# Kernel tuning notes

Hardware: AMD Instinct MI355X
Metric: run time of the kernel (lower is better)

## Reference

```python
import jax, jax.numpy as jnp
import numpy as np

T, B, D, H, DH = 2048, 2, 1024, 16, 64


def _rel_shift(x):
    # x: (Q, R, B, H) -- standard Transformer-XL relative shift via pad/reshape
    Q, R = x.shape[0], x.shape[1]
    zero_pad = jnp.zeros((Q, 1) + x.shape[2:], dtype=x.dtype)
    xp = jnp.concatenate([zero_pad, x], axis=1)          # (Q, R+1, B, H)
    xp = xp.reshape((R + 1, Q) + x.shape[2:])            # (R+1, Q, B, H)
    return xp[1:].reshape(x.shape)                       # (Q, R, B, H)


def setup_inputs() -> dict:
    key = jax.random.key(0)
    ks = jax.random.split(key, 7)
    w = jax.random.normal(ks[0], (T, B, D), dtype=jnp.float32)
    r = jax.random.normal(ks[1], (T, D), dtype=jnp.float32)
    w_qkv = jax.random.normal(ks[2], (3 * H * DH, D), dtype=jnp.float32) * 0.02
    w_r = jax.random.normal(ks[3], (H * DH, D), dtype=jnp.float32) * 0.02
    w_o = jax.random.normal(ks[4], (D, H * DH), dtype=jnp.float32) * 0.02
    r_r_bias = jax.random.normal(ks[5], (H, DH), dtype=jnp.float32) * 0.02
    attn_mask = jax.random.uniform(ks[6], (T, B)) < 0.1
    return {"w": w, "r": r, "w_qkv": w_qkv, "w_r": w_r, "w_o": w_o,
            "r_r_bias": r_r_bias, "attn_mask": attn_mask}


def reference(w, r, w_qkv, w_r, w_o, r_r_bias, attn_mask):
    qlen, bsz, d_model = w.shape
    n_head, d_head = r_r_bias.shape
    rlen = r.shape[0]
    scale = 1.0 / d_head ** 0.5

    heads = jnp.einsum('tbd,ed->tbe', w, w_qkv)           # (T, B, 3*H*DH)
    q, k, v = jnp.split(heads, 3, axis=-1)
    q = q.reshape(qlen, bsz, n_head, d_head)
    k = k.reshape(qlen, bsz, n_head, d_head)
    v = v.reshape(qlen, bsz, n_head, d_head)
    r_head_k = jnp.einsum('rd,ed->re', r, w_r).reshape(rlen, n_head, d_head)

    # NOTE: source uses r_r_bias for BOTH content and position biases
    rq = q + r_r_bias[None, None]                         # (Q, B, H, DH)
    AC = jnp.einsum('qbhd,kbhd->bhqk', rq, k)             # content scores
    BD = jnp.einsum('qbhd,rhd->bhqr', rq, r_head_k)       # position scores

    BD = jnp.transpose(BD, (2, 3, 0, 1))                  # (Q, R, B, H)
    BD = _rel_shift(BD)
    BD = jnp.transpose(BD, (2, 3, 0, 1))                  # (B, H, Q, R)
    BD = BD[:, :, :, :qlen]                               # klen == qlen

    score = (AC + BD) * scale                             # (B, H, Q, K)
    # key-padding mask (K, B) -> broadcast (B, 1, 1, K)
    score = jnp.where(attn_mask.T[:, None, None, :], -jnp.inf, score)

    prob = jax.nn.softmax(score.astype(jnp.float32), axis=-1).astype(score.dtype)
    attn_vec = jnp.einsum('bhqk,kbhd->qbhd', prob, v).reshape(qlen, bsz, n_head * d_head)
    out = jnp.einsum('qbe,de->qbd', attn_vec, w_o)        # (Q, B, D)
    return out, prob
```

## Files before the change

### kernel.cpp

```cpp
#include <hip/hip_runtime.h>
#include <hip/hip_bf16.h>
#include <cstdint>
#include <cstddef>

#define TLEN 2048
#define NB 2
#define DMODEL 1024
#define NH 16
#define NDH 64

typedef unsigned short ushortT;
typedef short bf16x8 __attribute__((ext_vector_type(8)));
typedef float f32x16 __attribute__((ext_vector_type(16)));

__device__ __forceinline__ ushortT f2bf(float f) {
  union { float f; unsigned int u; } x{f};
  unsigned int r = x.u + 0x7fff + ((x.u >> 16) & 1);
  return (ushortT)(r >> 16);
}
__device__ __forceinline__ unsigned int pk2(float lo, float hi) {
  return ((unsigned int)f2bf(hi) << 16) | (unsigned int)f2bf(lo);
}
__device__ __forceinline__ float bf2f(ushortT u) {
  union { unsigned int u; float f; } x;
  x.u = ((unsigned int)u) << 16;
  return x.f;
}

__device__ __forceinline__ void gld_lds16(const void* g, void* l) {
  __builtin_amdgcn_global_load_lds(
      (const __attribute__((address_space(1))) unsigned int*)g,
      (__attribute__((address_space(3))) unsigned int*)l, 16, 0, 0);
}


__global__ __launch_bounds__(256) void cvt_all(
    const float* __restrict__ w, const float* __restrict__ wqkv,
    const float* __restrict__ r, const float* __restrict__ wr,
    const float* __restrict__ wo, ushortT* __restrict__ w_bf,
    ushortT* __restrict__ wqkv_bf, ushortT* __restrict__ r_bf,
    ushortT* __restrict__ wr_bf, ushortT* __restrict__ wo_bf,
    const int* __restrict__ mask, float* __restrict__ mfl,
    ushortT* __restrict__ rkE) {
  const size_t N0 = 1048576, N1 = N0 + 786432, N2 = N1 + 524288,
               N3 = N2 + 262144, N4 = N3 + 262144;
  size_t i = (size_t)blockIdx.x * 256 + threadIdx.x;
  const float* src; ushortT* dst; size_t off;
  if (i < N0)      { src = w;    dst = w_bf;    off = i; }
  else if (i < N1) { src = wqkv; dst = wqkv_bf; off = i - N0; }
  else if (i < N2) { src = r;    dst = r_bf;    off = i - N1; }
  else if (i < N3) { src = wr;   dst = wr_bf;   off = i - N2; }
  else if (i < N4) { src = wo;   dst = wo_bf;   off = i - N3; }
  else {
    size_t k = i - N4;
    if (k < 512) {
      int j = (int)k * 4;
#pragma unroll
      for (int s = 0; s < 4; ++s) {
        mfl[j + s]        = mask[(size_t)(j + s) * NB]     ? 0.f : 1.f;
        mfl[TLEN + j + s] = mask[(size_t)(j + s) * NB + 1] ? 0.f : 1.f;
      }
    } else if (k < 512 + 256) {
      int ii = (int)k - 512; int h = ii >> 4, c = ii & 15;
      ushort4 z; z.x = 0; z.y = 0; z.z = 0; z.w = 0;
      *reinterpret_cast<ushort4*>(rkE + ((size_t)h * 4096 + 2048) * NDH + c * 4) = z;
    }
    return;
  }
  float4 v = reinterpret_cast<const float4*>(src)[off];
  ushort4 o;
  o.x = f2bf(v.x); o.y = f2bf(v.y); o.z = f2bf(v.z); o.w = f2bf(v.w);
  reinterpret_cast<ushort4*>(dst)[off] = o;
}


template <typename Epi>
__global__ __launch_bounds__(256) void gemm_bf16(const ushortT* __restrict__ A,
                                                 const ushortT* __restrict__ B,
                                                 int K, Epi epi) {
  __shared__ ushortT Al[128 * 64];
  __shared__ ushortT Bl[128 * 64];
  const int tid = threadIdx.x;
  const int lane = tid & 63;
  const int wv = tid >> 6;
  const int wm = wv >> 1, wn = wv & 1;
  const int m0 = blockIdx.y * 128;
  const int n0 = blockIdx.x * 128;
  const int r32 = lane & 31;
  const int hh = lane >> 5;

  f32x16 acc[2][2];
#pragma unroll
  for (int i = 0; i < 2; ++i)
#pragma unroll
    for (int j = 0; j < 2; ++j)
#pragma unroll
      for (int e = 0; e < 16; ++e) acc[i][j][e] = 0.f;

  for (int k0 = 0; k0 < K; k0 += 64) {
#pragma unroll
    for (int it = 0; it < 4; ++it) {
      int idx = it * 256 + tid;
      int r = idx >> 3, c = idx & 7;
      int gcol = k0 + ((c ^ (r & 7)) << 3);
      gld_lds16(A + (size_t)(m0 + r) * K + gcol, Al + idx * 8);
      gld_lds16(B + (size_t)(n0 + r) * K + gcol, Bl + idx * 8);
    }
    asm volatile("s_waitcnt vmcnt(0)");
    __syncthreads();
#pragma unroll
    for (int kc = 0; kc < 4; ++kc) {
      int lc = kc * 2 + hh;
      bf16x8 af[2], bfr[2];
#pragma unroll
      for (int f = 0; f < 2; ++f) {
        int ar = wm * 64 + f * 32 + r32;
        af[f] = *(const bf16x8*)(Al + ar * 64 + ((lc ^ (ar & 7)) << 3));
        int br = wn * 64 + f * 32 + r32;
        bfr[f] = *(const bf16x8*)(Bl + br * 64 + ((lc ^ (br & 7)) << 3));
      }
#pragma unroll
      for (int i = 0; i < 2; ++i)
#pragma unroll
        for (int j = 0; j < 2; ++j)
          acc[i][j] = __builtin_amdgcn_mfma_f32_32x32x16_bf16(af[i], bfr[j],
                                                              acc[i][j], 0, 0, 0);
    }
    __syncthreads();
  }

#pragma unroll
  for (int i = 0; i < 2; ++i)
#pragma unroll
    for (int j = 0; j < 2; ++j)
#pragma unroll
      for (int rg = 0; rg < 16; ++rg) {
        int m = m0 + wm * 64 + i * 32 + (rg & 3) + 8 * (rg >> 2) + 4 * hh;
        int n = n0 + wn * 64 + j * 32 + r32;
        epi.store(m, n, acc[i][j][rg]);
      }
}

struct EpiQKV {
  ushortT* qb; ushortT* kb; ushortT* vtb; const float* bias;
  __device__ void store(int m, int n, float val) const {
    int t = m >> 1, b = m & 1;
    int which = n >> 10;
    int h = (n >> 6) & (NH - 1);
    int dh = n & (NDH - 1);
    int bh = b * NH + h;
    if (which == 0)
      qb[((size_t)bh * TLEN + t) * NDH + dh] = f2bf(val + bias[(h << 6) | dh]);
    else if (which == 1)
      kb[((size_t)bh * TLEN + t) * NDH + dh] = f2bf(val);
    else
      vtb[((size_t)bh * NDH + dh) * TLEN + t] = f2bf(val);
  }
};

struct EpiRK {
  ushortT* rkE;
  __device__ void store(int m, int n, float val) const {
    int h = n >> 6, dh = n & 63;
    ushortT v = f2bf(val);
    rkE[((size_t)h * 4096 + m) * NDH + dh] = v;
    if (m <= 2046)
      rkE[((size_t)h * 4096 + m + 2049) * NDH + dh] = v;
  }
};

struct EpiOut {
  float* out;
  __device__ void store(int m, int n, float val) const {
    out[(size_t)m * DMODEL + n] = val;
  }
};


__global__ __launch_bounds__(128) void attn_fast(
    const ushortT* __restrict__ qb, const ushortT* __restrict__ kb,
    const ushortT* __restrict__ vtb, const ushortT* __restrict__ rkE,
    const float* __restrict__ mfl, unsigned int* __restrict__ S,
    float* __restrict__ linv_g, ushortT* __restrict__ av_bf) {
  __shared__ float W[2][64][32];
  __shared__ ushortT KT[2048];
  __shared__ ushortT VT[2048];
  __shared__ ushortT RK[6144];

  const int bh = blockIdx.y;
  const int b = bh >> 4, h = bh & 15;
  const int t = threadIdx.x >> 6;
  const int lane = threadIdx.x & 63;
  const int ql = lane & 31;
  const int hh = lane >> 5;
  const int Q0 = blockIdx.x * 64;
  const int q0 = Q0 + 32 * t;
  const int qg = q0 + ql;

  const ushortT* Qbh = qb + (size_t)bh * TLEN * NDH;
  const ushortT* Kbh = kb + (size_t)bh * TLEN * NDH;
  const ushortT* Vbh = vtb + (size_t)bh * NDH * TLEN;
  const ushortT* Rh  = rkE + (size_t)h * 4096 * NDH;
  const float* mflb  = mfl + (size_t)b * TLEN;
  unsigned int* Sb   = S + (size_t)bh * (TLEN / 2) * TLEN;
  float (*Wp)[32] = W[t];

  auto STAGE = [&](int j0) {
    const int U = 1984 + j0 - Q0;
#pragma unroll
    for (int i = 0; i < 6; ++i) {
      int ci = (t * 6 + i) * 64 + lane;
      int row = ci >> 3, c = ci & 7;
      gld_lds16(Rh + (size_t)(U + row) * NDH + ((c ^ (row & 7)) << 3), RK + ci * 8);
    }
#pragma unroll
    for (int i = 0; i < 2; ++i) {
      int ci = (t * 2 + i) * 64 + lane;
      int row = ci >> 3, c = ci & 7;
      gld_lds16(Kbh + (size_t)(j0 + row) * NDH + ((c ^ (row & 7)) << 3), KT + ci * 8);
      int d = ci >> 2, c2 = ci & 3;
      gld_lds16(Vbh + (size_t)d * TLEN + j0 + ((c2 ^ (d & 3)) << 3), VT + ci * 8);
    }
  };

  bf16x8 Qf[4], Qs[4];
  {
    int r2 = min(qg + 1, TLEN - 1);
#pragma unroll
    for (int c = 0; c < 4; ++c) {
      Qf[c] = *(const bf16x8*)(Qbh + (size_t)qg * NDH + c * 16 + hh * 8);
      Qs[c] = *(const bf16x8*)(Qbh + (size_t)r2 * NDH + c * 16 + hh * 8);
    }
  }

  f32x16 pacc0, pacc1;
#pragma unroll
  for (int i = 0; i < 16; ++i) { pacc0[i] = 0.f; pacc1[i] = 0.f; }
  float l_acc = 0.f;

  STAGE(0);
  asm volatile("s_waitcnt vmcnt(0)");
  __builtin_amdgcn_s_barrier();

  for (int j0 = 0; j0 < TLEN; j0 += 32) {
    float4 mf4[4];
#pragma unroll
    for (int g = 0; g < 4; ++g)
      mf4[g] = *(const float4*)(mflb + j0 + 8 * g + 4 * hh);

    const int R1 = 32 * (1 - t) + ql;
    const int R2 = R1 + 32;
    bf16x8 a1[4], a2[4], ak[4];
#pragma unroll
    for (int c = 0; c < 4; ++c) {
      a1[c] = *(const bf16x8*)(RK + R1 * 64 + (((2 * c + hh) ^ (R1 & 7)) << 3));
      a2[c] = *(const bf16x8*)(RK + R2 * 64 + (((2 * c + hh) ^ (R2 & 7)) << 3));
      ak[c] = *(const bf16x8*)(KT + ql * 64 + (((2 * c + hh) ^ (ql & 7)) << 3));
    }
    bf16x8 vv0[2], vv1[2];
#pragma unroll
    for (int kh = 0; kh < 2; ++kh) {
      vv0[kh] = *(const bf16x8*)(VT + ql * 32 + (((2 * kh + hh) ^ (ql & 3)) << 3));
      vv1[kh] = *(const bf16x8*)(VT + (32 + ql) * 32 + (((2 * kh + hh) ^ (ql & 3)) << 3));
    }
    asm volatile("s_waitcnt lgkmcnt(0)");
    __builtin_amdgcn_s_barrier();

    if (j0 + 32 < TLEN) STAGE(j0 + 32);

    const bool t0w1 = (j0 <= q0);
    const bool t1w1 = (j0 < q0);

    f32x16 facc;
#pragma unroll
    for (int i = 0; i < 16; ++i) facc[i] = 0.f;
    __builtin_amdgcn_s_setprio(1);
#pragma unroll
    for (int c = 0; c < 4; ++c)
      facc = __builtin_amdgcn_mfma_f32_32x32x16_bf16(a1[c], t0w1 ? Qf[c] : Qs[c], facc, 0, 0, 0);
    __builtin_amdgcn_s_setprio(0);
#pragma unroll
    for (int r = 0; r < 16; ++r)
      Wp[(r & 3) + 8 * (r >> 2) + 4 * hh][ql] = facc[r];

#pragma unroll
    for (int i = 0; i < 16; ++i) facc[i] = 0.f;
    __builtin_amdgcn_s_setprio(1);
#pragma unroll
    for (int c = 0; c < 4; ++c)
      facc = __builtin_amdgcn_mfma_f32_32x32x16_bf16(a2[c], t1w1 ? Qf[c] : Qs[c], facc, 0, 0, 0);
    __builtin_amdgcn_s_setprio(0);
#pragma unroll
    for (int r = 0; r < 16; ++r)
      Wp[32 + (r & 3) + 8 * (r >> 2) + 4 * hh][ql] = facc[r];

    f32x16 cacc;
#pragma unroll
    for (int i = 0; i < 16; ++i) cacc[i] = 0.f;
    __builtin_amdgcn_s_setprio(1);
#pragma unroll
    for (int c = 0; c < 4; ++c)
      cacc = __builtin_amdgcn_mfma_f32_32x32x16_bf16(ak[c], Qf[c], cacc, 0, 0, 0);
    __builtin_amdgcn_s_setprio(0);

    float p[16];
#pragma unroll
    for (int r = 0; r < 16; ++r) {
      int jrow = (r & 3) + 8 * (r >> 2) + 4 * hh;
      float bd = Wp[jrow - ql + 31][ql];
      float sc = (cacc[r] + bd) * 0.125f;
      float mv = (&mf4[r >> 2].x)[r & 3];
      float pv = mv * __expf(sc);
      p[r] = pv;
      l_acc += pv;
    }

    unsigned int u[8];
#pragma unroll
    for (int i = 0; i < 8; ++i) u[i] = pk2(p[2 * i], p[2 * i + 1]);

#pragma unroll
    for (int i = 0; i < 8; ++i) {
      int r = 2 * i;
      int jrow = (r & 3) + 8 * (r >> 2) + 4 * hh;
      Sb[(size_t)((j0 + jrow) >> 1) * TLEN + qg] = u[i];
    }

#pragma unroll
    for (int kh = 0; kh < 2; ++kh) {
      unsigned int t0 = (unsigned int)__shfl_xor((int)u[4 * kh + 0], 32);
      unsigned int t1 = (unsigned int)__shfl_xor((int)u[4 * kh + 1], 32);
      unsigned int t2 = (unsigned int)__shfl_xor((int)u[4 * kh + 2], 32);
      unsigned int t3 = (unsigned int)__shfl_xor((int)u[4 * kh + 3], 32);
      unsigned int fr[4];
      fr[0] = hh ? t2 : u[4 * kh + 0];
      fr[1] = hh ? t3 : u[4 * kh + 1];
      fr[2] = hh ? u[4 * kh + 2] : t0;
      fr[3] = hh ? u[4 * kh + 3] : t1;
      bf16x8 pa = *reinterpret_cast<bf16x8*>(fr);
      __builtin_amdgcn_s_setprio(1);
      pacc0 = __builtin_amdgcn_mfma_f32_32x32x16_bf16(pa, kh ? vv0[1] : vv0[0], pacc0, 0, 0, 0);
      pacc1 = __builtin_amdgcn_mfma_f32_32x32x16_bf16(pa, kh ? vv1[1] : vv1[0], pacc1, 0, 0, 0);
      __builtin_amdgcn_s_setprio(0);
    }

    if (j0 + 32 < TLEN) {
      asm volatile("s_waitcnt vmcnt(8)");
      __builtin_amdgcn_s_barrier();
    }
  }

  float lt = l_acc + __shfl_xor(l_acc, 32);
  if (lane < 32) linv_g[(size_t)bh * TLEN + qg] = 1.0f / lt;
  float inv = 1.0f / lt;
#pragma unroll
  for (int r = 0; r < 16; ++r) {
    int qrow = (r & 3) + 8 * (r >> 2) + 4 * hh;
    float iv = __shfl(inv, qrow);
    size_t aoff = ((size_t)(q0 + qrow) * NB + b) * DMODEL + h * NDH;
    av_bf[aoff + ql] = f2bf(pacc0[r] * iv);
    av_bf[aoff + 32 + ql] = f2bf(pacc1[r] * iv);
  }
}


__global__ __launch_bounds__(256) void rescale_t(const unsigned int* __restrict__ S,
                                                 const float* __restrict__ linv_g,
                                                 float* __restrict__ prob) {
  __shared__ unsigned int lds[64][65];
  __shared__ float liv[64];
  const int qt = blockIdx.x;
  const int jt = blockIdx.y;
  const int bh = blockIdx.z;
  const int t = threadIdx.x;

  const unsigned int* Sb = S + ((size_t)bh * (TLEN / 2) + jt * 64) * TLEN + qt * 64;
  {
    int row = t >> 2, c0 = (t & 3) * 16;
#pragma unroll
    for (int k = 0; k < 4; ++k) {
      uint4 v = *reinterpret_cast<const uint4*>(Sb + (size_t)row * TLEN + c0 + k * 4);
      lds[row][c0 + k * 4 + 0] = v.x;
      lds[row][c0 + k * 4 + 1] = v.y;
      lds[row][c0 + k * 4 + 2] = v.z;
      lds[row][c0 + k * 4 + 3] = v.w;
    }
  }
  if (t < 64) liv[t] = linv_g[(size_t)bh * TLEN + qt * 64 + t];
  __syncthreads();

  float* P = prob + ((size_t)bh * TLEN + qt * 64) * TLEN + jt * 128;
#pragma unroll
  for (int k = 0; k < 8; ++k) {
    int idx = k * 256 + t;
    int row = idx >> 5, c4 = idx & 31;
    unsigned int u0 = lds[c4 * 2][row];
    unsigned int u1 = lds[c4 * 2 + 1][row];
    float iv = liv[row];
    float4 o;
    o.x = bf2f((ushortT)(u0 & 0xffff)) * iv;
    o.y = bf2f((ushortT)(u0 >> 16)) * iv;
    o.z = bf2f((ushortT)(u1 & 0xffff)) * iv;
    o.w = bf2f((ushortT)(u1 >> 16)) * iv;
    *reinterpret_cast<float4*>(P + (size_t)row * TLEN + c4 * 4) = o;
  }
}


__global__ __launch_bounds__(256) void attn_fused(
    const ushortT* __restrict__ qb, const ushortT* __restrict__ kb,
    const ushortT* __restrict__ vtb, const ushortT* __restrict__ rkE,
    const float* __restrict__ mfl, float* __restrict__ prob,
    ushortT* __restrict__ av_bf) {
  __shared__ float W[4][64][32];
  __shared__ float sl[4][32];
  __shared__ float linv[64];

  const int bh = blockIdx.y;
  const int b = bh >> 4, h = bh & 15;
  const int wv = threadIdx.x >> 6;
  const int lane = threadIdx.x & 63;
  const int ql = lane & 31;
  const int hh = lane >> 5;
  const int qtile = wv & 1;
  const int jh = wv >> 1;
  const int q0 = blockIdx.x * 64 + qtile * 32;
  const int qg = q0 + ql;

  const ushortT* Qbh = qb + (size_t)bh * TLEN * NDH;
  const ushortT* Kbh = kb + (size_t)bh * TLEN * NDH;
  const ushortT* Vbh = vtb + (size_t)bh * NDH * TLEN;
  const ushortT* Rh  = rkE + (size_t)h * 4096 * NDH;
  const float* mflb  = mfl + (size_t)b * TLEN;
  float (*Wp)[32] = W[wv];

  bf16x8 Qf[4], Qs[4];
  {
    int r2 = min(qg + 1, TLEN - 1);
#pragma unroll
    for (int c = 0; c < 4; ++c) {
      Qf[c] = *(const bf16x8*)(Qbh + (size_t)qg * NDH + c * 16 + hh * 8);
      Qs[c] = *(const bf16x8*)(Qbh + (size_t)r2 * NDH + c * 16 + hh * 8);
    }
  }

  f32x16 pacc0, pacc1;
#pragma unroll
  for (int i = 0; i < 16; ++i) { pacc0[i] = 0.f; pacc1[i] = 0.f; }
  float l_acc = 0.f;

  ushortT* pbrow = (ushortT*)prob + ((size_t)bh * TLEN + qg) * 4096 + 2048;

  const int jbeg = jh * (TLEN / 2);
  const int jend = jbeg + (TLEN / 2);
  for (int j0 = jbeg; j0 < jend; j0 += 32) {
    const int base_t = 2016 + j0 - q0;
    const bool t0w1 = (j0 <= q0);
    const bool t1w1 = (j0 < q0);

    const ushortT* s0 = Rh + (size_t)(base_t + ql) * NDH + hh * 8;
    const ushortT* s1 = Rh + (size_t)(base_t + 32 + ql) * NDH + hh * 8;
    const ushortT* sk = Kbh + (size_t)(j0 + ql) * NDH + hh * 8;
    const ushortT* vrow0 = Vbh + (size_t)ql * TLEN + j0 + 8 * hh;
    const ushortT* vrow1 = Vbh + (size_t)(32 + ql) * TLEN + j0 + 8 * hh;
    bf16x8 rk0[4], rk1[4], kk[4];
#pragma unroll
    for (int c = 0; c < 4; ++c) {
      rk0[c] = *(const bf16x8*)(s0 + c * 16);
      rk1[c] = *(const bf16x8*)(s1 + c * 16);
      kk[c]  = *(const bf16x8*)(sk + c * 16);
    }
    bf16x8 v00 = *(const bf16x8*)(vrow0);
    bf16x8 v01 = *(const bf16x8*)(vrow0 + 16);
    bf16x8 v10 = *(const bf16x8*)(vrow1);
    bf16x8 v11 = *(const bf16x8*)(vrow1 + 16);
    float4 mf4[4];
#pragma unroll
    for (int g = 0; g < 4; ++g)
      mf4[g] = *(const float4*)(mflb + j0 + 8 * g + 4 * hh);

    f32x16 facc;
#pragma unroll
    for (int i = 0; i < 16; ++i) facc[i] = 0.f;
    __builtin_amdgcn_s_setprio(1);
#pragma unroll
    for (int c = 0; c < 4; ++c)
      facc = __builtin_amdgcn_mfma_f32_32x32x16_bf16(rk0[c], t0w1 ? Qf[c] : Qs[c], facc, 0, 0, 0);
    __builtin_amdgcn_s_setprio(0);
#pragma unroll
    for (int r = 0; r < 16; ++r)
      Wp[(r & 3) + 8 * (r >> 2) + 4 * hh][ql] = facc[r];

#pragma unroll
    for (int i = 0; i < 16; ++i) facc[i] = 0.f;
    __builtin_amdgcn_s_setprio(1);
#pragma unroll
    for (int c = 0; c < 4; ++c)
      facc = __builtin_amdgcn_mfma_f32_32x32x16_bf16(rk1[c], t1w1 ? Qf[c] : Qs[c], facc, 0, 0, 0);
    __builtin_amdgcn_s_setprio(0);
#pragma unroll
    for (int r = 0; r < 16; ++r)
      Wp[32 + (r & 3) + 8 * (r >> 2) + 4 * hh][ql] = facc[r];

    f32x16 cacc;
#pragma unroll
    for (int i = 0; i < 16; ++i) cacc[i] = 0.f;
    __builtin_amdgcn_s_setprio(1);
#pragma unroll
    for (int c = 0; c < 4; ++c)
      cacc = __builtin_amdgcn_mfma_f32_32x32x16_bf16(kk[c], Qf[c], cacc, 0, 0, 0);
    __builtin_amdgcn_s_setprio(0);

    float p[16];
#pragma unroll
    for (int r = 0; r < 16; ++r) {
      int jrow = (r & 3) + 8 * (r >> 2) + 4 * hh;
      float bd = Wp[jrow - ql + 31][ql];
      float sc = (cacc[r] + bd) * 0.125f;
      float mv = (&mf4[r >> 2].x)[r & 3];
      float pv = mv * __expf(sc);
      p[r] = pv;
      l_acc += pv;
    }

#pragma unroll
    for (int g = 0; g < 4; ++g) {
      uint2 st;
      st.x = pk2(p[4 * g + 0], p[4 * g + 1]);
      st.y = pk2(p[4 * g + 2], p[4 * g + 3]);
      *reinterpret_cast<uint2*>(pbrow + j0 + 8 * g + 4 * hh) = st;
    }

#pragma unroll
    for (int kh = 0; kh < 2; ++kh) {
      unsigned int u0 = pk2(p[8 * kh + 0], p[8 * kh + 1]);
      unsigned int u1 = pk2(p[8 * kh + 2], p[8 * kh + 3]);
      unsigned int u2 = pk2(p[8 * kh + 4], p[8 * kh + 5]);
      unsigned int u3 = pk2(p[8 * kh + 6], p[8 * kh + 7]);
      unsigned int t0 = (unsigned int)__shfl_xor((int)u0, 32);
      unsigned int t1 = (unsigned int)__shfl_xor((int)u1, 32);
      unsigned int t2 = (unsigned int)__shfl_xor((int)u2, 32);
      unsigned int t3 = (unsigned int)__shfl_xor((int)u3, 32);
      unsigned int fr[4];
      fr[0] = hh ? t2 : u0;
      fr[1] = hh ? t3 : u1;
      fr[2] = hh ? u2 : t0;
      fr[3] = hh ? u3 : t1;
      bf16x8 pa = *reinterpret_cast<bf16x8*>(fr);
      __builtin_amdgcn_s_setprio(1);
      pacc0 = __builtin_amdgcn_mfma_f32_32x32x16_bf16(pa, kh ? v01 : v00, pacc0, 0, 0, 0);
      pacc1 = __builtin_amdgcn_mfma_f32_32x32x16_bf16(pa, kh ? v11 : v10, pacc1, 0, 0, 0);
      __builtin_amdgcn_s_setprio(0);
    }
  }

#pragma unroll
  for (int r = 0; r < 16; ++r) {
    int qrow = (r & 3) + 8 * (r >> 2) + 4 * hh;
    Wp[qrow][ql] = pacc0[r];
    Wp[32 + qrow][ql] = pacc1[r];
  }
  float lh = l_acc + __shfl_xor(l_acc, 32);
  if (lane < 32) sl[wv][ql] = lh;
  __syncthreads();

  if (wv < 2) {
    if (lane < 32) {
      float lt = sl[wv][ql] + sl[wv + 2][ql];
      linv[wv * 32 + ql] = 1.0f / lt;
    }
#pragma unroll
    for (int r = 0; r < 16; ++r) {
      int qrow = (r & 3) + 8 * (r >> 2) + 4 * hh;
      float lt = sl[wv][qrow] + sl[wv + 2][qrow];
      float iv = 1.0f / lt;
      float s0v = W[wv][qrow][ql] + W[wv + 2][qrow][ql];
      float s1v = W[wv][32 + qrow][ql] + W[wv + 2][32 + qrow][ql];
      size_t aoff = ((size_t)(q0 + qrow) * NB + b) * DMODEL + h * NDH;
      av_bf[aoff + ql] = f2bf(s0v * iv);
      av_bf[aoff + 32 + ql] = f2bf(s1v * iv);
    }
  }
  __syncthreads();

  const ushortT* probus = (const ushortT*)prob;
  const int lr = lane >> 4;
  const int cg = lane & 15;
  for (int s = 0; s < 8; ++s) {
    const int rloc = qtile * 32 + s * 4 + lr;
    const int rowg = blockIdx.x * 64 + rloc;
    const size_t ub = ((size_t)bh * TLEN + rowg) * 4096 + 2048 + jh * 1024 + cg * 8;
    const size_t fb = ((size_t)bh * TLEN + rowg) * 2048 + jh * 1024 + cg * 8;
    uint4 a[8];
#pragma unroll
    for (int k = 0; k < 8; ++k)
      a[k] = *reinterpret_cast<const uint4*>(probus + ub + k * 128);
    const float iv = linv[rloc];
    __syncthreads();
#pragma unroll
    for (int k = 0; k < 8; ++k) {
      float4 o0, o1;
      o0.x = bf2f((ushortT)(a[k].x & 0xffff)) * iv;
      o0.y = bf2f((ushortT)(a[k].x >> 16)) * iv;
      o0.z = bf2f((ushortT)(a[k].y & 0xffff)) * iv;
      o0.w = bf2f((ushortT)(a[k].y >> 16)) * iv;
      o1.x = bf2f((ushortT)(a[k].z & 0xffff)) * iv;
      o1.y = bf2f((ushortT)(a[k].z >> 16)) * iv;
      o1.z = bf2f((ushortT)(a[k].w & 0xffff)) * iv;
      o1.w = bf2f((ushortT)(a[k].w >> 16)) * iv;
      *reinterpret_cast<float4*>(prob + fb + k * 128) = o0;
      *reinterpret_cast<float4*>(prob + fb + k * 128 + 4) = o1;
    }
  }
}


extern "C" void kernel_launch(void* const* d_in, const int* in_sizes, int n_in,
                              void* d_out, int out_size, void* d_ws, size_t ws_size,
                              hipStream_t stream) {
  const float* w      = (const float*)d_in[0];
  const float* r      = (const float*)d_in[1];
  const float* w_qkv  = (const float*)d_in[2];
  const float* w_r    = (const float*)d_in[3];
  const float* w_o    = (const float*)d_in[4];
  const float* bias   = (const float*)d_in[5];
  const int* mask     = (const int*)d_in[6];

  float* out  = (float*)d_out;
  float* prob = out + (size_t)TLEN * NB * DMODEL;

  const size_t SZ = (size_t)NB * NH * TLEN * NDH;
  ushortT* w_bf    = (ushortT*)d_ws;
  ushortT* wqkv_bf = w_bf + (size_t)4096 * 1024;
  ushortT* r_bf    = wqkv_bf + (size_t)3072 * 1024;
  ushortT* wr_bf   = r_bf + (size_t)2048 * 1024;
  ushortT* wo_bf   = wr_bf + (size_t)1024 * 1024;
  ushortT* q_bf    = wo_bf + (size_t)1024 * 1024;
  ushortT* k_bf    = q_bf + SZ;
  ushortT* vt_bf   = k_bf + SZ;
  ushortT* rkE_bf  = vt_bf + SZ;
  ushortT* av_bf   = rkE_bf + (size_t)NH * 4096 * NDH;
  float* mfl       = (float*)(av_bf + SZ);
  float* linv_g    = mfl + (size_t)NB * TLEN;
  unsigned int* S  = (unsigned int*)(linv_g + (size_t)NB * NH * TLEN);
  const size_t need = (size_t)((char*)(S + (size_t)NB * NH * (TLEN / 2) * TLEN) -
                               (char*)d_ws);
  const bool fast = ws_size >= need;

  cvt_all<<<dim3((2883584 + 768 + 255) / 256), 256, 0, stream>>>(
      w, w_qkv, r, w_r, w_o, w_bf, wqkv_bf, r_bf, wr_bf, wo_bf, mask, mfl, rkE_bf);

  EpiQKV e1{q_bf, k_bf, vt_bf, bias};
  gemm_bf16<EpiQKV><<<dim3(3072 / 128, 4096 / 128), 256, 0, stream>>>(w_bf, wqkv_bf, DMODEL, e1);
  EpiRK e2{rkE_bf};
  gemm_bf16<EpiRK><<<dim3(1024 / 128, 2048 / 128), 256, 0, stream>>>(r_bf, wr_bf, DMODEL, e2);

  if (fast) {
    attn_fast<<<dim3(32, 32), 128, 0, stream>>>(q_bf, k_bf, vt_bf, rkE_bf,
                                                mfl, S, linv_g, av_bf);
    rescale_t<<<dim3(32, 16, 32), 256, 0, stream>>>(S, linv_g, prob);
  } else {
    attn_fused<<<dim3(32, 32), 256, 0, stream>>>(q_bf, k_bf, vt_bf, rkE_bf,
                                                 mfl, prob, av_bf);
  }

  EpiOut e5{out};
  gemm_bf16<EpiOut><<<dim3(1024 / 128, 4096 / 128), 256, 0, stream>>>(av_bf, wo_bf, DMODEL, e5);
}
```

Measured before the change: 445.4 us.

## Overlap GEMM tile loads with MFMA and remap attention blocks per XCD

The bf16 GEMM now reads a whole K-tile's fragments into registers, barriers, then issues the global-to-LDS load for the next tile before running the MFMAs under raised wave priority. This hides global load latency behind compute using a single LDS buffer. Separately, attention blocks are remapped so that each XCD handles a contiguous set of (batch, head) pairs, which should improve L2 reuse of K/V/R data. The change costs extra registers for fragments, which may reduce occupancy.

```diff
diff --git a/kernel.cpp b/kernel.cpp
--- a/kernel.cpp
+++ b/kernel.cpp
@@ -89,15 +89,7 @@
   const int r32 = lane & 31;
   const int hh = lane >> 5;
 
-  f32x16 acc[2][2];
-#pragma unroll
-  for (int i = 0; i < 2; ++i)
-#pragma unroll
-    for (int j = 0; j < 2; ++j)
-#pragma unroll
-      for (int e = 0; e < 16; ++e) acc[i][j][e] = 0.f;
-
-  for (int k0 = 0; k0 < K; k0 += 64) {
+  auto STAGE = [&](int k0) {
 #pragma unroll
     for (int it = 0; it < 4; ++it) {
       int idx = it * 256 + tid;
@@ -106,27 +98,53 @@
       gld_lds16(A + (size_t)(m0 + r) * K + gcol, Al + idx * 8);
       gld_lds16(B + (size_t)(n0 + r) * K + gcol, Bl + idx * 8);
     }
-    asm volatile("s_waitcnt vmcnt(0)");
-    __syncthreads();
+  };
+
+  f32x16 acc[2][2];
+#pragma unroll
+  for (int i = 0; i < 2; ++i)
+#pragma unroll
+    for (int j = 0; j < 2; ++j)
+#pragma unroll
+      for (int e = 0; e < 16; ++e) acc[i][j][e] = 0.f;
+
+  STAGE(0);
+  asm volatile("s_waitcnt vmcnt(0)");
+  __builtin_amdgcn_s_barrier();
+
+  for (int k0 = 0; k0 < K; k0 += 64) {
+    bf16x8 af[4][2], bfr[4][2];
 #pragma unroll
     for (int kc = 0; kc < 4; ++kc) {
       int lc = kc * 2 + hh;
-      bf16x8 af[2], bfr[2];
 #pragma unroll
       for (int f = 0; f < 2; ++f) {
         int ar = wm * 64 + f * 32 + r32;
-        af[f] = *(const bf16x8*)(Al + ar * 64 + ((lc ^ (ar & 7)) << 3));
+        af[kc][f] = *(const bf16x8*)(Al + ar * 64 + ((lc ^ (ar & 7)) << 3));
         int br = wn * 64 + f * 32 + r32;
-        bfr[f] = *(const bf16x8*)(Bl + br * 64 + ((lc ^ (br & 7)) << 3));
+        bfr[kc][f] = *(const bf16x8*)(Bl + br * 64 + ((lc ^ (br & 7)) << 3));
       }
+    }
+    asm volatile("s_waitcnt lgkmcnt(0)");
+    __builtin_amdgcn_s_barrier();
+
+    if (k0 + 64 < K) STAGE(k0 + 64);
+
+    __builtin_amdgcn_s_setprio(1);
+#pragma unroll
+    for (int kc = 0; kc < 4; ++kc)
 #pragma unroll
       for (int i = 0; i < 2; ++i)
 #pragma unroll
         for (int j = 0; j < 2; ++j)
-          acc[i][j] = __builtin_amdgcn_mfma_f32_32x32x16_bf16(af[i], bfr[j],
+          acc[i][j] = __builtin_amdgcn_mfma_f32_32x32x16_bf16(af[kc][i], bfr[kc][j],
                                                               acc[i][j], 0, 0, 0);
-    }
-    __syncthreads();
+    __builtin_amdgcn_s_setprio(0);
+
+    if (k0 + 64 < K) {
+      asm volatile("s_waitcnt vmcnt(0)");
+      __builtin_amdgcn_s_barrier();
+    }
   }
 
 #pragma unroll
@@ -187,13 +205,18 @@
   __shared__ ushortT VT[2048];
   __shared__ ushortT RK[6144];
 
-  const int bh = blockIdx.y;
+  const int flat = blockIdx.y * 32 + blockIdx.x;
+  const int xcd = flat & 7;
+  const int idx = flat >> 3;
+  const int bh = xcd * 4 + (idx >> 5);
+  const int qt = idx & 31;
+
   const int b = bh >> 4, h = bh & 15;
   const int t = threadIdx.x >> 6;
   const int lane = threadIdx.x & 63;
   const int ql = lane & 31;
   const int hh = lane >> 5;
-  const int Q0 = blockIdx.x * 64;
+  const int Q0 = qt * 64;
   const int q0 = Q0 + 32 * t;
   const int qg = q0 + ql;
 
```

Result: slower. 461.9 us (+3.7%).
